# Kernel tuning notes

Measured on AMD Instinct MI355X. Metric: run time of the kernel, lower is better.

The kernel has to match this reference:

```python
import jax, jax.numpy as jnp
import numpy as np

N = 4096   # patients
D = 256    # encoding dim per modality
EPS = 1e-8 # torch CosineSimilarity eps


def setup_inputs() -> dict:
    key = jax.random.key(0)
    ks = jax.random.split(key, 7)
    return {
        "log_hazard": jax.random.normal(ks[0], (N,), dtype=jnp.float32),
        "time": jax.random.randint(ks[1], (N,), 0, 3650, dtype=jnp.int32),
        "event": jax.random.randint(ks[2], (N,), 0, 2, dtype=jnp.int32),
        "eb0": jax.random.normal(ks[3], (N, D), dtype=jnp.float32),
        "eb1": jax.random.normal(ks[4], (N, D), dtype=jnp.float32),
        "eb2": jax.random.normal(ks[5], (N, D), dtype=jnp.float32),
        "eb3": jax.random.normal(ks[6], (N, D), dtype=jnp.float32),
        "M_margin": 1,
    }


def _cox_npll(h, t, e):
    # risk_matrix = (outer(t,t) >= t^2).T  ->  risk[i,j] = (t_j * t_i >= t_i^2)
    tt = t[:, None] * t[None, :]                      # [N,N] = t_i * t_j
    risk = (tt >= (t * t)[:, None]).astype(h.dtype)   # row i: patients j with t_j >= t_i
    log_denom = jnp.log(risk @ jnp.exp(h))            # [N]
    ef = e.astype(h.dtype)
    return -jnp.sum(ef * (h - log_denom)) / jnp.sum(ef)


def _similarity_loss(blocks, margin):
    # Vectorized form of the O(N^2 * n_mod) pairwise loop.
    matched = jnp.zeros((N, N), dtype=blocks[0].dtype)  # sum_mod cos(x_i, x_j) over valid mods
    own = jnp.zeros((N, N), dtype=blocks[0].dtype)      # sum_mod cos(x_i, x_i) over valid mods
    for x in blocks:
        nrm = jnp.linalg.norm(x, axis=1)                # [N]
        den = jnp.maximum(nrm, EPS)
        xn = x / den[:, None]
        S = xn @ xn.T                                   # cos(x_i, x_j) with torch eps semantics
        diag = (nrm * nrm) / (den * den)                # cos(x_i, x_i)
        miss = jnp.all(x == x[:, :1], axis=1)           # modality missing (constant row)
        valid = (~(miss[:, None] | miss[None, :])).astype(x.dtype)
        matched = matched + valid * S
        own = own + valid * diag[:, None]
    offdiag = 1.0 - jnp.eye(N, dtype=matched.dtype)
    per_pair = jax.nn.relu(margin - matched + own)
    return jnp.sum(offdiag * per_pair)


def reference(log_hazard, time, event, eb0, eb1, eb2, eb3, M_margin):
    margin = jnp.float32(M_margin)
    cox = _cox_npll(log_hazard, time, event)
    sim = _similarity_loss([eb0, eb1, eb2, eb3], margin)
    return cox + sim
```

## Files before the change

kernel.cpp:

```cpp
#include <hip/hip_runtime.h>
#include <stdint.h>

#define NPAT 4096
#define DIM  256
#define EPSV 1e-8f
#define BT   128
#define NT   (NPAT / BT)
#define NBLK (NT * (NT + 1) / 2)
#define NSTEP 16
#define NBINS 4096

typedef float f32x4  __attribute__((ext_vector_type(4)));
typedef float f32x16 __attribute__((ext_vector_type(16)));
typedef int   i32x4  __attribute__((ext_vector_type(4)));
typedef int   i32x8  __attribute__((ext_vector_type(8)));

#define WS_DVAL_OFF 256
#define WS_MVEC_OFF (WS_DVAL_OFF + 16*NPAT)
#define WS_XN_OFF   (WS_MVEC_OFF + 16*NPAT)

__device__ __forceinline__ float decode_margin(const int* pm) {
  int v = *pm;
  if (v > -16777216 && v < 16777216) return (float)v;
  return __int_as_float(v);
}

__device__ __forceinline__ i32x8 ld_op(const uint8_t* p) {
  union { i32x8 w; i32x4 h[2]; } u;
  u.h[0] = *(const i32x4*)(p);
  u.h[1] = *(const i32x4*)(p + 1024);
  return u.w;
}

__global__ __launch_bounds__(256) void prep_kernel(
    const float4* __restrict__ eb0, const float4* __restrict__ eb1,
    const float4* __restrict__ eb2, const float4* __restrict__ eb3,
    uint8_t* __restrict__ XnF, float* __restrict__ dval_f,
    float* __restrict__ mvec_f, float* __restrict__ scal)
{
  const int i    = blockIdx.x;
  const int wv   = threadIdx.x >> 6;
  const int lane = threadIdx.x & 63;
  const float4* ebs[4] = {eb0, eb1, eb2, eb3};
  const float4 v = ebs[wv][i * (DIM / 4) + lane];
  float s = v.x * v.x + v.y * v.y + v.z * v.z + v.w * v.w;
#pragma unroll
  for (int o = 32; o; o >>= 1) s += __shfl_down(s, o, 64);
  s = __shfl(s, 0, 64);
  const float x0 = __shfl(v.x, 0, 64);
  const bool eq = (v.x == x0) && (v.y == x0) && (v.z == x0) && (v.w == x0);
  const bool miss = (__ballot(eq) == ~0ull);
  const float nrm = sqrtf(s);
  const float den = fmaxf(nrm, EPSV);
  const float inv = miss ? 0.0f : (1.0f / den);
  int p = 0;
  p = __builtin_amdgcn_cvt_pk_fp8_f32(v.x * inv, v.y * inv, p, false);
  p = __builtin_amdgcn_cvt_pk_fp8_f32(v.z * inv, v.w * inv, p, true);
  const int g  = i >> 5, r = i & 31;
  const int ss = wv * 4 + (lane >> 4);
  const int h  = (lane >> 3) & 1;
  const int q  = (lane >> 2) & 1;
  const int b16 = (lane & 3) * 4;
  *(int*)&XnF[(size_t)(g * 16 + ss) * 2048 + q * 1024 +
              (size_t)(h * 32 + r) * 16 + b16] = p;
  if (lane == 0) {
    const float diag = (nrm * nrm) / (den * den);
    dval_f[i * 4 + wv] = miss ? 0.0f : diag;
    mvec_f[i * 4 + wv] = miss ? 0.0f : 1.0f;
  }
  if (i == 0 && threadIdx.x == 0) {
    scal[0] = 0.0f;
    scal[1] = 0.0f;
    ((unsigned*)scal)[2] = 0u;
  }
}

__global__ __launch_bounds__(256, 3) void sim_gemm_kernel(
    const uint8_t* __restrict__ XnF, const float4* __restrict__ dval,
    const float4* __restrict__ mvec, const int* __restrict__ pmargin,
    const float* __restrict__ h, const int* __restrict__ t,
    const int* __restrict__ e, float* __restrict__ scal,
    float* __restrict__ out)
{
  __shared__ __align__(16) uint8_t smem[32768 + 256];
  const int L   = blockIdx.x;
  const int tid = threadIdx.x;
  const int lane = tid & 63, wvv = tid >> 6;

  if (L == 0) {
    float* bins = (float*)smem;
    float* wt   = (float*)(smem + 16384);
    float* rn   = (float*)(smem + 16384 + 32);
    float* rd   = (float*)(smem + 16384 + 64);
#pragma unroll
    for (int k = 0; k < 16; ++k) bins[tid + k * 256] = 0.0f;
    __syncthreads();
#pragma unroll
    for (int k = 0; k < 16; ++k) {
      const int i = tid + k * 256;
      atomicAdd(&bins[t[i]], expf(h[i]));
    }
    __syncthreads();
    float seg[16]; float part = 0.0f;
#pragma unroll
    for (int k = 0; k < 16; ++k) { seg[k] = bins[tid * 16 + k]; part += seg[k]; }
    float sfx = part;
#pragma unroll
    for (int off = 1; off < 64; off <<= 1) {
      const float u = __shfl_down(sfx, off, 64);
      if (lane + off < 64) sfx += u;
    }
    if (lane == 0) wt[wvv] = sfx;
    __syncthreads();
    float above = 0.0f;
    for (int w = wvv + 1; w < 4; ++w) above += wt[w];
    float run = above + (sfx - part);
#pragma unroll
    for (int k = 15; k >= 0; --k) { run += seg[k]; bins[tid * 16 + k] = run; }
    __syncthreads();
    float nloc = 0.0f, dloc = 0.0f;
#pragma unroll
    for (int k = 0; k < 16; ++k) {
      const int i = tid + k * 256;
      const float ei = (float)e[i];
      if (ei != 0.0f) { nloc += ei * (h[i] - logf(bins[t[i]])); dloc += ei; }
    }
#pragma unroll
    for (int o = 32; o; o >>= 1) {
      nloc += __shfl_down(nloc, o, 64);
      dloc += __shfl_down(dloc, o, 64);
    }
    if (lane == 0) { rn[wvv] = nloc; rd[wvv] = dloc; }
    __syncthreads();
    if (tid == 0) {
      float n = 0.0f, d = 0.0f;
#pragma unroll
      for (int k = 0; k < 4; ++k) { n += rn[k]; d += rd[k]; }
      atomicExch(&scal[1], n / d);
      __threadfence();
      const unsigned old = atomicAdd(&((unsigned*)scal)[2], 1u);
      if (old == NBLK) {
        __threadfence();
        out[0] = atomicAdd(&scal[0], 0.0f) - (n / d);
      }
    }
    return;
  }

  const int T = L - 1;
  int bi = (int)((2 * NT + 1 - sqrtf((float)((2 * NT + 1) * (2 * NT + 1)) - 8.0f * T)) * 0.5f);
  if (bi < 0) bi = 0;
  if (bi > NT - 1) bi = NT - 1;
  while (bi > 0 && bi * NT - bi * (bi - 1) / 2 > T) --bi;
  while ((bi + 1) * NT - (bi + 1) * bi / 2 <= T) ++bi;
  const int bj = bi + (T - (bi * NT - bi * (bi - 1) / 2));

  const int wi = wvv >> 1, wj = wvv & 1;
  const bool isDiag = (bi == bj);

#define STAGE(BUFOFF, S) do {                                                        \
    if (!isDiag || wvv < 2) {                                                        \
      _Pragma("unroll")                                                              \
      for (int t_ = 0; t_ < 4; ++t_) {                                               \
        const int ii = wvv * 4 + t_;                                                 \
        const int grp = (ii < 8) ? (bi * 4 + (ii >> 1)) : (bj * 4 + ((ii >> 1) & 3));\
        const uint8_t* src = XnF + (size_t)(grp * 16 + (S)) * 2048                   \
                             + (ii & 1) * 1024 + lane * 16;                          \
        uint8_t* dst = (uint8_t*)smem + (BUFOFF) + ii * 1024;                        \
        __builtin_amdgcn_global_load_lds(                                            \
            (const __attribute__((address_space(1))) unsigned int*)src,              \
            (__attribute__((address_space(3))) unsigned int*)dst, 16, 0, 0);         \
      }                                                                              \
    }                                                                                \
  } while (0)

  f32x16 acc[2][2] = {};

  STAGE(0, 0);
  int cur = 0;
#pragma unroll 1
  for (int s = 0; s < NSTEP; ++s) {
    if (s + 1 < NSTEP) STAGE((cur ^ 1) * 16384, s + 1);
    __syncthreads();
    const uint8_t* aB = (const uint8_t*)smem + cur * 16384 + (size_t)lane * 16;
    const uint8_t* bB = aB + (isDiag ? 0 : 8192);
    const i32x8 a0 = ld_op(aB + (wi * 2 + 0) * 2048);
    const i32x8 a1 = ld_op(aB + (wi * 2 + 1) * 2048);
    const i32x8 b0 = ld_op(bB + (wj * 2 + 0) * 2048);
    const i32x8 b1 = ld_op(bB + (wj * 2 + 1) * 2048);
    acc[0][0] = __builtin_amdgcn_mfma_scale_f32_32x32x64_f8f6f4(
        a0, b0, acc[0][0], 0, 0, 0, 0x7F7F7F7F, 0, 0x7F7F7F7F);
    acc[0][1] = __builtin_amdgcn_mfma_scale_f32_32x32x64_f8f6f4(
        a0, b1, acc[0][1], 0, 0, 0, 0x7F7F7F7F, 0, 0x7F7F7F7F);
    acc[1][0] = __builtin_amdgcn_mfma_scale_f32_32x32x64_f8f6f4(
        a1, b0, acc[1][0], 0, 0, 0, 0x7F7F7F7F, 0, 0x7F7F7F7F);
    acc[1][1] = __builtin_amdgcn_mfma_scale_f32_32x32x64_f8f6f4(
        a1, b1, acc[1][1], 0, 0, 0, 0x7F7F7F7F, 0, 0x7F7F7F7F);
    __syncthreads();
    cur ^= 1;
  }
#undef STAGE

  float4* eRDi = (float4*)smem;
  float4* eCMi = (float4*)smem + BT;
  float4* eRDj = (float4*)smem + 2 * BT;
  float4* eCMj = (float4*)smem + 3 * BT;
  float*  wred = (float*)(smem + 8192);
  if (tid < BT) {
    eRDi[tid] = dval[bi * BT + tid];
    eCMi[tid] = mvec[bi * BT + tid];
  } else {
    const int ss = tid - BT;
    eRDj[ss] = dval[bj * BT + ss];
    eCMj[ss] = mvec[bj * BT + ss];
  }
  __syncthreads();

  const float margin = decode_margin(pmargin);
  float local = 0.0f;
  const int colA = lane & 31, hsel = lane >> 5;
#pragma unroll
  for (int mi = 0; mi < 2; ++mi) {
#pragma unroll
    for (int mj = 0; mj < 2; ++mj) {
      const int jl = wj * 64 + mj * 32 + colA;
      const float4 cmj = eCMj[jl];
      const float4 rdj = eRDj[jl];
#pragma unroll
      for (int rr = 0; rr < 16; ++rr) {
        const int il = wi * 64 + mi * 32 + (rr & 3) + 8 * (rr >> 2) + 4 * hsel;
        const float4 rdi = eRDi[il];
        const float sv = acc[mi][mj][rr];
        const float own_ij = rdi.x * cmj.x + rdi.y * cmj.y + rdi.z * cmj.z + rdi.w * cmj.w;
        const float v1 = fmaxf(margin - sv + own_ij, 0.0f);
        local += (isDiag && il == jl) ? 0.0f : v1;
        if (!isDiag) {
          const float4 cmi = eCMi[il];
          const float own_ji = rdj.x * cmi.x + rdj.y * cmi.y + rdj.z * cmi.z + rdj.w * cmi.w;
          local += fmaxf(margin - sv + own_ji, 0.0f);
        }
      }
    }
  }
#pragma unroll
  for (int o = 32; o; o >>= 1) local += __shfl_down(local, o, 64);
  if (lane == 0) wred[wvv] = local;
  __syncthreads();
  if (tid == 0) {
    atomicAdd(&scal[0], wred[0] + wred[1] + wred[2] + wred[3]);
    __threadfence();
    const unsigned old = atomicAdd(&((unsigned*)scal)[2], 1u);
    if (old == NBLK) {
      __threadfence();
      out[0] = atomicAdd(&scal[0], 0.0f) - atomicAdd(&scal[1], 0.0f);
    }
  }
}

extern "C" void kernel_launch(void* const* d_in, const int* in_sizes, int n_in,
                              void* d_out, int out_size, void* d_ws, size_t ws_size,
                              hipStream_t stream) {
  const float* h    = (const float*)d_in[0];
  const int*   t    = (const int*)  d_in[1];
  const int*   e    = (const int*)  d_in[2];
  const float4* eb0 = (const float4*)d_in[3];
  const float4* eb1 = (const float4*)d_in[4];
  const float4* eb2 = (const float4*)d_in[5];
  const float4* eb3 = (const float4*)d_in[6];
  const int*   pm   = (const int*)  d_in[7];

  char*    ws   = (char*)d_ws;
  float*   scal = (float*)ws;
  float*   dvf  = (float*)(ws + WS_DVAL_OFF);
  float*   mvf  = (float*)(ws + WS_MVEC_OFF);
  uint8_t* XnF  = (uint8_t*)(ws + WS_XN_OFF);

  prep_kernel<<<NPAT, 256, 0, stream>>>(eb0, eb1, eb2, eb3, XnF, dvf, mvf, scal);
  sim_gemm_kernel<<<NBLK + 1, 256, 0, stream>>>(XnF, (const float4*)dvf, (const float4*)mvf,
                                                pm, h, t, e, scal, (float*)d_out);
}
```

Before: 111.1 us.

## Collapse double-buffered GEMM loop to one barrier per step with explicit waitcnts

Restructures the FP8 MFMA main loop so each step issues the next stage's global-to-LDS loads, reads operands from the current buffer, and ends with a single vmcnt wait plus s_barrier, replacing the two __syncthreads per step. Staging source and destination addresses are precomputed once outside the loop, and the loop is unrolled by two with the buffer index derived from the step parity. The intent is to cut barrier and address-computation overhead and let the prefetch overlap the MFMAs. Correctness now rests on the hand-placed waitcnt and barrier ordering; the next prefetch writes the other buffer, which was last read in the previous step, before that step's barrier.

```diff
diff --git a/kernel.cpp b/kernel.cpp
--- a/kernel.cpp
+++ b/kernel.cpp
@@ -157,37 +157,49 @@
 
   const int wi = wvv >> 1, wj = wvv & 1;
   const bool isDiag = (bi == bj);
-
-#define STAGE(BUFOFF, S) do {                                                        \
-    if (!isDiag || wvv < 2) {                                                        \
-      _Pragma("unroll")                                                              \
-      for (int t_ = 0; t_ < 4; ++t_) {                                               \
-        const int ii = wvv * 4 + t_;                                                 \
-        const int grp = (ii < 8) ? (bi * 4 + (ii >> 1)) : (bj * 4 + ((ii >> 1) & 3));\
-        const uint8_t* src = XnF + (size_t)(grp * 16 + (S)) * 2048                   \
-                             + (ii & 1) * 1024 + lane * 16;                          \
-        uint8_t* dst = (uint8_t*)smem + (BUFOFF) + ii * 1024;                        \
-        __builtin_amdgcn_global_load_lds(                                            \
-            (const __attribute__((address_space(1))) unsigned int*)src,              \
-            (__attribute__((address_space(3))) unsigned int*)dst, 16, 0, 0);         \
-      }                                                                              \
+  const bool doStage = (!isDiag || wvv < 2);
+
+  const uint8_t* src0[4];
+  int dofs[4];
+#pragma unroll
+  for (int t_ = 0; t_ < 4; ++t_) {
+    const int ii = wvv * 4 + t_;
+    const int grp = (ii < 8) ? (bi * 4 + (ii >> 1)) : (bj * 4 + ((ii >> 1) & 3));
+    src0[t_] = XnF + (size_t)(grp * 16) * 2048 + (ii & 1) * 1024 + (size_t)lane * 16;
+    dofs[t_] = ii * 1024;
+  }
+
+#define STAGE(BUFOFF, S) do { if (doStage) {                                         \
+    _Pragma("unroll")                                                                \
+    for (int t_ = 0; t_ < 4; ++t_) {                                                 \
+      __builtin_amdgcn_global_load_lds(                                              \
+          (const __attribute__((address_space(1))) unsigned int*)                    \
+              (src0[t_] + (size_t)(S) * 2048),                                       \
+          (__attribute__((address_space(3))) unsigned int*)                          \
+              ((uint8_t*)smem + (BUFOFF) + dofs[t_]), 16, 0, 0);                     \
     }                                                                                \
-  } while (0)
+  } } while (0)
 
   f32x16 acc[2][2] = {};
 
   STAGE(0, 0);
-  int cur = 0;
-#pragma unroll 1
+  asm volatile("s_waitcnt vmcnt(0)" ::: "memory");
+  __builtin_amdgcn_sched_barrier(0);
+  __builtin_amdgcn_s_barrier();
+  __builtin_amdgcn_sched_barrier(0);
+
+#pragma unroll 2
   for (int s = 0; s < NSTEP; ++s) {
-    if (s + 1 < NSTEP) STAGE((cur ^ 1) * 16384, s + 1);
-    __syncthreads();
-    const uint8_t* aB = (const uint8_t*)smem + cur * 16384 + (size_t)lane * 16;
+    const int cb = (s & 1) * 16384;
+    if (s + 1 < NSTEP) STAGE(((s + 1) & 1) * 16384, s + 1);
+    const uint8_t* aB = (const uint8_t*)smem + cb + (size_t)lane * 16;
     const uint8_t* bB = aB + (isDiag ? 0 : 8192);
-    const i32x8 a0 = ld_op(aB + (wi * 2 + 0) * 2048);
-    const i32x8 a1 = ld_op(aB + (wi * 2 + 1) * 2048);
-    const i32x8 b0 = ld_op(bB + (wj * 2 + 0) * 2048);
-    const i32x8 b1 = ld_op(bB + (wj * 2 + 1) * 2048);
+    const i32x8 a0 = ld_op(aB + wi * 4096);
+    const i32x8 a1 = ld_op(aB + wi * 4096 + 2048);
+    const i32x8 b0 = ld_op(bB + wj * 4096);
+    const i32x8 b1 = ld_op(bB + wj * 4096 + 2048);
+    asm volatile("s_waitcnt lgkmcnt(0)" ::: "memory");
+    __builtin_amdgcn_sched_barrier(0);
     acc[0][0] = __builtin_amdgcn_mfma_scale_f32_32x32x64_f8f6f4(
         a0, b0, acc[0][0], 0, 0, 0, 0x7F7F7F7F, 0, 0x7F7F7F7F);
     acc[0][1] = __builtin_amdgcn_mfma_scale_f32_32x32x64_f8f6f4(
@@ -196,8 +208,10 @@
         a1, b0, acc[1][0], 0, 0, 0, 0x7F7F7F7F, 0, 0x7F7F7F7F);
     acc[1][1] = __builtin_amdgcn_mfma_scale_f32_32x32x64_f8f6f4(
         a1, b1, acc[1][1], 0, 0, 0, 0x7F7F7F7F, 0, 0x7F7F7F7F);
-    __syncthreads();
-    cur ^= 1;
+    asm volatile("s_waitcnt vmcnt(0)" ::: "memory");
+    __builtin_amdgcn_sched_barrier(0);
+    __builtin_amdgcn_s_barrier();
+    __builtin_amdgcn_sched_barrier(0);
   }
 #undef STAGE
 
```

Result: no change. 112.3 us (+1.1%).
